# Kernel tuning notes

Hardware: AMD Instinct MI355X
Metric: run time of the kernel (lower is better)

The kernel has to match this reference:

```python
import jax, jax.numpy as jnp
import numpy as np

D = 1024
H = 16
HD = D // H
B = 4
L = 2048
FFN = 4 * D
EPS = 1e-5


def _layer_norm(x, g, b):
    mu = jnp.mean(x, axis=-1, keepdims=True)
    var = jnp.mean(jnp.square(x - mu), axis=-1, keepdims=True)
    return (x - mu) * jax.lax.rsqrt(var + EPS) * g + b


def setup_inputs() -> dict:
    key = jax.random.key(0)
    ks = jax.random.split(key, 16)
    s = 1.0 / np.sqrt(D)
    inp = {
        "x": jax.random.normal(ks[0], (B, L, D), dtype=jnp.float32),
        "rel_pos_bias": jax.random.normal(ks[1], (1, H, L, L), dtype=jnp.float32) * 0.02,
        "wq": jax.random.normal(ks[2], (D, D), dtype=jnp.float32) * s,
        "bq": jnp.zeros((D,), jnp.float32),
        "wk": jax.random.normal(ks[3], (D, D), dtype=jnp.float32) * s,
        "bk": jnp.zeros((D,), jnp.float32),
        "wv": jax.random.normal(ks[4], (D, D), dtype=jnp.float32) * s,
        "bv": jnp.zeros((D,), jnp.float32),
        "wo": jax.random.normal(ks[5], (D, D), dtype=jnp.float32) * s,
        "bo": jnp.zeros((D,), jnp.float32),
        "g1": jnp.ones((D,), jnp.float32),
        "be1": jnp.zeros((D,), jnp.float32),
        "g2": jnp.ones((D,), jnp.float32),
        "be2": jnp.zeros((D,), jnp.float32),
        "w1": jax.random.normal(ks[6], (D, FFN), dtype=jnp.float32) * s,
        "bf1": jnp.zeros((FFN,), jnp.float32),
        "w2": jax.random.normal(ks[7], (FFN, D), dtype=jnp.float32) * (1.0 / np.sqrt(FFN)),
        "bf2": jnp.zeros((D,), jnp.float32),
    }
    return inp


def reference(x, rel_pos_bias, wq, bq, wk, bk, wv, bv, wo, bo,
              g1, be1, g2, be2, w1, bf1, w2, bf2):
    scale = HD ** -0.5
    residual = x
    xn = _layer_norm(x, g1, be1)
    # projections -> (B, H, L, HD)
    q = (xn @ wq + bq).reshape(B, L, H, HD).transpose(0, 2, 1, 3)
    k = (xn @ wk + bk).reshape(B, L, H, HD).transpose(0, 2, 1, 3)
    v = (xn @ wv + bv).reshape(B, L, H, HD).transpose(0, 2, 1, 3)
    scores = jnp.einsum('bhqd,bhkd->bhqk', q, k) * scale
    causal = jnp.tril(jnp.ones((L, L), dtype=bool))
    scores = jnp.where(causal[None, None], scores, -jnp.inf)
    scores = scores + rel_pos_bias
    attn = jax.nn.softmax(scores, axis=-1)
    out = jnp.einsum('bhqk,bhkd->bhqd', attn, v)
    out = out.transpose(0, 2, 1, 3).reshape(B, L, D)
    out = out @ wo + bo
    x = residual + out
    residual = x
    xn = _layer_norm(x, g2, be2)
    h = jax.nn.relu(xn @ w1 + bf1)
    x = residual + (h @ w2 + bf2)
    return x
```

## Files before the change

### kernel.cpp

```cpp
#include <hip/hip_runtime.h>
#include <hip/hip_bf16.h>

#define D_   1024
#define H_   16
#define HD_  64
#define B_   4
#define L_   2048
#define FFN_ 4096
#define M_   (B_ * L_)

typedef __bf16 bf16x8 __attribute__((ext_vector_type(8)));
typedef float f32x4 __attribute__((ext_vector_type(4)));
typedef unsigned short ushort8 __attribute__((ext_vector_type(8)));
typedef unsigned short ushort4v __attribute__((ext_vector_type(4)));

__device__ inline unsigned short f2bf(float f) {
    unsigned int u = __float_as_uint(f);
    u += 0x7fff + ((u >> 16) & 1);
    return (unsigned short)(u >> 16);
}
__device__ inline float bf2f(unsigned short u) {
    return __uint_as_float(((unsigned int)u) << 16);
}

__global__ __launch_bounds__(256) void k_transpose_bf16(
    const float* __restrict__ in, unsigned short* __restrict__ out, int K, int N)
{
    __shared__ float tile[64][65];
    int k0 = blockIdx.y * 64, n0 = blockIdx.x * 64;
    int t = threadIdx.x;
    int r = t >> 2, cs = (t & 3) * 16;
    const float* src = in + (size_t)(k0 + r) * N + n0 + cs;
#pragma unroll
    for (int i = 0; i < 16; i += 4) {
        float4 v = *(const float4*)(src + i);
        tile[r][cs + i + 0] = v.x;
        tile[r][cs + i + 1] = v.y;
        tile[r][cs + i + 2] = v.z;
        tile[r][cs + i + 3] = v.w;
    }
    __syncthreads();
    unsigned short* dst = out + (size_t)(n0 + r) * K + k0 + cs;
#pragma unroll
    for (int i = 0; i < 16; ++i) dst[i] = f2bf(tile[cs + i][r]);
}

__global__ void k_concat_bias(const float* __restrict__ bq, const float* __restrict__ bk,
                              const float* __restrict__ bv, float* __restrict__ out)
{
    int i = blockIdx.x * 256 + threadIdx.x;
    float v = (i < 1024) ? bq[i] : (i < 2048 ? bk[i - 1024] : bv[i - 2048]);
    out[i] = v;
}

__global__ __launch_bounds__(256) void k_layernorm(
    const float* __restrict__ x, const float* __restrict__ g, const float* __restrict__ be,
    unsigned short* __restrict__ out)
{
    int row = blockIdx.x;
    const float* xr = x + (size_t)row * D_;
    int t = threadIdx.x;
    float4 v = *(const float4*)(xr + t * 4);
    float s = v.x + v.y + v.z + v.w;
    float sq = v.x * v.x + v.y * v.y + v.z * v.z + v.w * v.w;
#pragma unroll
    for (int off = 32; off >= 1; off >>= 1) {
        s  += __shfl_down(s, off);
        sq += __shfl_down(sq, off);
    }
    __shared__ float ps[4], psq[4];
    int w = t >> 6;
    if ((t & 63) == 0) { ps[w] = s; psq[w] = sq; }
    __syncthreads();
    float tot  = ps[0] + ps[1] + ps[2] + ps[3];
    float totq = psq[0] + psq[1] + psq[2] + psq[3];
    float mu  = tot * (1.f / D_);
    float var = totq * (1.f / D_) - mu * mu;
    float inv = rsqrtf(var + 1e-5f);
    float4 gv = *(const float4*)(g + t * 4);
    float4 bv = *(const float4*)(be + t * 4);
    ushort4v o;
    o[0] = f2bf((v.x - mu) * inv * gv.x + bv.x);
    o[1] = f2bf((v.y - mu) * inv * gv.y + bv.y);
    o[2] = f2bf((v.z - mu) * inv * gv.z + bv.z);
    o[3] = f2bf((v.w - mu) * inv * gv.w + bv.w);
    *(ushort4v*)(out + (size_t)row * D_ + t * 4) = o;
}

template <bool OUT_BF16, bool RELU, bool RESID>
__global__ __launch_bounds__(256, 2) void k_gemm(
    const unsigned short* __restrict__ A, const unsigned short* __restrict__ Bt,
    const float* __restrict__ bias, const float* __restrict__ resid,
    void* __restrict__ Cout, int M, int N, int K)
{
    __shared__ unsigned short sA[128 * 40];
    __shared__ unsigned short sB[128 * 40];
    int m0 = blockIdx.y * 128, n0 = blockIdx.x * 128;
    int tid = threadIdx.x, lane = tid & 63, wvi = tid >> 6;
    int wm = (wvi & 1) * 64, wn = (wvi >> 1) * 64;
    int lr = lane & 15, qd = lane >> 4;

    f32x4 acc[4][4] = {};

    int sr = tid >> 2, ss = (tid & 3) * 8;
    const unsigned short* pA0 = A  + (size_t)(m0 + sr)      * K + ss;
    const unsigned short* pA1 = A  + (size_t)(m0 + 64 + sr) * K + ss;
    const unsigned short* pB0 = Bt + (size_t)(n0 + sr)      * K + ss;
    const unsigned short* pB1 = Bt + (size_t)(n0 + 64 + sr) * K + ss;

    for (int k0 = 0; k0 < K; k0 += 32) {
        ushort8 a0 = *(const ushort8*)(pA0 + k0);
        ushort8 a1 = *(const ushort8*)(pA1 + k0);
        ushort8 b0 = *(const ushort8*)(pB0 + k0);
        ushort8 b1 = *(const ushort8*)(pB1 + k0);
        if (k0) __syncthreads();
        *(ushort8*)(sA + sr * 40 + ss)        = a0;
        *(ushort8*)(sA + (64 + sr) * 40 + ss) = a1;
        *(ushort8*)(sB + sr * 40 + ss)        = b0;
        *(ushort8*)(sB + (64 + sr) * 40 + ss) = b1;
        __syncthreads();
        bf16x8 af[4], bfr[4];
#pragma unroll
        for (int i = 0; i < 4; ++i)
            af[i] = *(const bf16x8*)(sA + (wm + i * 16 + lr) * 40 + qd * 8);
#pragma unroll
        for (int i = 0; i < 4; ++i)
            bfr[i] = *(const bf16x8*)(sB + (wn + i * 16 + lr) * 40 + qd * 8);
#pragma unroll
        for (int mi = 0; mi < 4; ++mi)
#pragma unroll
            for (int ni = 0; ni < 4; ++ni)
                acc[mi][ni] = __builtin_amdgcn_mfma_f32_16x16x32_bf16(
                    af[mi], bfr[ni], acc[mi][ni], 0, 0, 0);
    }

#pragma unroll
    for (int ni = 0; ni < 4; ++ni) {
        int col = n0 + wn + ni * 16 + lr;
        float bvv = bias[col];
#pragma unroll
        for (int mi = 0; mi < 4; ++mi) {
#pragma unroll
            for (int r = 0; r < 4; ++r) {
                int row = m0 + wm + mi * 16 + qd * 4 + r;
                float v = acc[mi][ni][r] + bvv;
                if (RELU) v = fmaxf(v, 0.f);
                if (RESID) v += resid[(size_t)row * N + col];
                if (OUT_BF16)
                    ((unsigned short*)Cout)[(size_t)row * N + col] = f2bf(v);
                else
                    ((float*)Cout)[(size_t)row * N + col] = v;
            }
        }
    }
}

__global__ __launch_bounds__(256, 2) void k_attn(
    const unsigned short* __restrict__ qkv, const float* __restrict__ rpb,
    unsigned short* __restrict__ out)
{
    __shared__ unsigned short Qs[64 * 72];
    __shared__ unsigned short Ks[64 * 72];
    __shared__ unsigned short Vt[64 * 72];
    __shared__ unsigned short Sp[64 * 72];
    int h = blockIdx.x >> 2, b = blockIdx.x & 3;
    int q0 = blockIdx.y * 64;
    int t = threadIdx.x, lane = t & 63, w = t >> 6;
    int lr = lane & 15, qd = lane >> 4;
    int sr = t >> 2, ss = (t & 3) * 16;

    {
        const unsigned short* src = qkv + (size_t)(b * L_ + q0 + sr) * 3072 + h * 64 + ss;
        *(ushort8*)(Qs + sr * 72 + ss)     = *(const ushort8*)src;
        *(ushort8*)(Qs + sr * 72 + ss + 8) = *(const ushort8*)(src + 8);
    }

    f32x4 oacc[4] = {};
    float m_r[4], l_r[4];
#pragma unroll
    for (int r = 0; r < 4; ++r) { m_r[r] = -1e30f; l_r[r] = 0.f; }

    int ntile = q0 / 64 + 1;
    for (int kt = 0; kt < ntile; ++kt) {
        int k0 = kt * 64;
        __syncthreads();
        const unsigned short* ksrc = qkv + (size_t)(b * L_ + k0 + sr) * 3072 + 1024 + h * 64 + ss;
        *(ushort8*)(Ks + sr * 72 + ss)     = *(const ushort8*)ksrc;
        *(ushort8*)(Ks + sr * 72 + ss + 8) = *(const ushort8*)(ksrc + 8);
        const unsigned short* vsrc = qkv + (size_t)(b * L_ + k0 + sr) * 3072 + 2048 + h * 64 + ss;
        ushort8 v0 = *(const ushort8*)vsrc;
        ushort8 v1 = *(const ushort8*)(vsrc + 8);
#pragma unroll
        for (int i = 0; i < 8; ++i) Vt[(ss + i) * 72 + sr] = v0[i];
#pragma unroll
        for (int i = 0; i < 8; ++i) Vt[(ss + 8 + i) * 72 + sr] = v1[i];
        __syncthreads();

        f32x4 sc[4] = {};
#pragma unroll
        for (int ks = 0; ks < 2; ++ks) {
            bf16x8 aq = *(const bf16x8*)(Qs + (w * 16 + lr) * 72 + ks * 32 + qd * 8);
#pragma unroll
            for (int nt = 0; nt < 4; ++nt) {
                bf16x8 bk8 = *(const bf16x8*)(Ks + (nt * 16 + lr) * 72 + ks * 32 + qd * 8);
                sc[nt] = __builtin_amdgcn_mfma_f32_16x16x32_bf16(aq, bk8, sc[nt], 0, 0, 0);
            }
        }

        int qrow_base = q0 + w * 16 + qd * 4;
        const float* rpb_base = rpb + ((size_t)h * L_ + qrow_base) * L_ + k0;
        float pvv[4][4], mx[4];
#pragma unroll
        for (int r = 0; r < 4; ++r) {
            mx[r] = -1e30f;
#pragma unroll
            for (int nt = 0; nt < 4; ++nt) {
                int kcol = k0 + nt * 16 + lr;
                float sv = sc[nt][r] * 0.125f + rpb_base[(size_t)r * L_ + nt * 16 + lr];
                if (kcol > qrow_base + r) sv = -1e30f;
                pvv[r][nt] = sv;
                mx[r] = fmaxf(mx[r], sv);
            }
        }
#pragma unroll
        for (int r = 0; r < 4; ++r) {
            mx[r] = fmaxf(mx[r], __shfl_xor(mx[r], 1));
            mx[r] = fmaxf(mx[r], __shfl_xor(mx[r], 2));
            mx[r] = fmaxf(mx[r], __shfl_xor(mx[r], 4));
            mx[r] = fmaxf(mx[r], __shfl_xor(mx[r], 8));
        }
#pragma unroll
        for (int r = 0; r < 4; ++r) {
            float mnew  = fmaxf(m_r[r], mx[r]);
            float alpha = __expf(m_r[r] - mnew);
            float psum = 0.f;
#pragma unroll
            for (int nt = 0; nt < 4; ++nt) {
                float p = __expf(pvv[r][nt] - mnew);
                psum += p;
                Sp[(w * 16 + qd * 4 + r) * 72 + nt * 16 + lr] = f2bf(p);
            }
            psum += __shfl_xor(psum, 1);
            psum += __shfl_xor(psum, 2);
            psum += __shfl_xor(psum, 4);
            psum += __shfl_xor(psum, 8);
            l_r[r] = l_r[r] * alpha + psum;
            m_r[r] = mnew;
            oacc[0][r] *= alpha; oacc[1][r] *= alpha;
            oacc[2][r] *= alpha; oacc[3][r] *= alpha;
        }

#pragma unroll
        for (int ks = 0; ks < 2; ++ks) {
            bf16x8 ap = *(const bf16x8*)(Sp + (w * 16 + lr) * 72 + ks * 32 + qd * 8);
#pragma unroll
            for (int dt = 0; dt < 4; ++dt) {
                bf16x8 bv8 = *(const bf16x8*)(Vt + (dt * 16 + lr) * 72 + ks * 32 + qd * 8);
                oacc[dt] = __builtin_amdgcn_mfma_f32_16x16x32_bf16(ap, bv8, oacc[dt], 0, 0, 0);
            }
        }
    }

#pragma unroll
    for (int r = 0; r < 4; ++r) {
        float linv = 1.f / l_r[r];
        int qrow = q0 + w * 16 + qd * 4 + r;
        unsigned short* dst = out + (size_t)(b * L_ + qrow) * 1024 + h * 64;
#pragma unroll
        for (int dt = 0; dt < 4; ++dt)
            dst[dt * 16 + lr] = f2bf(oacc[dt][r] * linv);
    }
}

extern "C" void kernel_launch(void* const* d_in, const int* in_sizes, int n_in,
                              void* d_out, int out_size, void* d_ws, size_t ws_size,
                              hipStream_t stream)
{
    const float* x   = (const float*)d_in[0];
    const float* rpb = (const float*)d_in[1];
    const float* wq  = (const float*)d_in[2];
    const float* bq  = (const float*)d_in[3];
    const float* wk  = (const float*)d_in[4];
    const float* bk  = (const float*)d_in[5];
    const float* wv  = (const float*)d_in[6];
    const float* bv  = (const float*)d_in[7];
    const float* wo  = (const float*)d_in[8];
    const float* bo  = (const float*)d_in[9];
    const float* g1  = (const float*)d_in[10];
    const float* be1 = (const float*)d_in[11];
    const float* g2  = (const float*)d_in[12];
    const float* be2 = (const float*)d_in[13];
    const float* w1  = (const float*)d_in[14];
    const float* bf1 = (const float*)d_in[15];
    const float* w2  = (const float*)d_in[16];
    const float* bf2 = (const float*)d_in[17];
    float* out = (float*)d_out;
    char* ws = (char*)d_ws;

    unsigned short* xn1   = (unsigned short*)(ws + 0);
    unsigned short* qkv   = (unsigned short*)(ws + 16777216);
    unsigned short* attno = (unsigned short*)(ws + 0);
    unsigned short* hbuf  = (unsigned short*)(ws + 0);
    float*          xmid  = (float*)(ws + 67108864);
    unsigned short* xn2   = (unsigned short*)(ws + 100663296);
    unsigned short* wqkvT = (unsigned short*)(ws + 117440512);
    unsigned short* woT   = (unsigned short*)(ws + 123731968);
    unsigned short* w1T   = (unsigned short*)(ws + 125829120);
    unsigned short* w2T   = (unsigned short*)(ws + 134217728);
    float*          bqkv  = (float*)(ws + 142606336);

    k_transpose_bf16<<<dim3(16, 16), 256, 0, stream>>>(wq, wqkvT,                1024, 1024);
    k_transpose_bf16<<<dim3(16, 16), 256, 0, stream>>>(wk, wqkvT + 1024 * 1024,  1024, 1024);
    k_transpose_bf16<<<dim3(16, 16), 256, 0, stream>>>(wv, wqkvT + 2048 * 1024,  1024, 1024);
    k_transpose_bf16<<<dim3(16, 16), 256, 0, stream>>>(wo, woT,                  1024, 1024);
    k_transpose_bf16<<<dim3(64, 16), 256, 0, stream>>>(w1, w1T,                  1024, 4096);
    k_transpose_bf16<<<dim3(16, 64), 256, 0, stream>>>(w2, w2T,                  4096, 1024);
    k_concat_bias<<<12, 256, 0, stream>>>(bq, bk, bv, bqkv);

    k_layernorm<<<M_, 256, 0, stream>>>(x, g1, be1, xn1);
    k_gemm<true, false, false><<<dim3(24, 64), 256, 0, stream>>>(
        xn1, wqkvT, bqkv, nullptr, qkv, M_, 3072, 1024);
    k_attn<<<dim3(64, 32), 256, 0, stream>>>(qkv, rpb, attno);
    k_gemm<false, false, true><<<dim3(8, 64), 256, 0, stream>>>(
        attno, woT, bo, x, xmid, M_, 1024, 1024);
    k_layernorm<<<M_, 256, 0, stream>>>(xmid, g2, be2, xn2);
    k_gemm<true, true, false><<<dim3(32, 64), 256, 0, stream>>>(
        xn2, w1T, bf1, nullptr, hbuf, M_, 4096, 1024);
    k_gemm<false, false, true><<<dim3(8, 64), 256, 0, stream>>>(
        hbuf, w2T, bf2, xmid, out, M_, 1024, 4096);
}
```

Baseline: 1.023 ms.

## Restructure attention to share bias across batches; direct-to-LDS GEMM loads

The attention kernel now runs one 512-thread block per head and query tile, with its eight waves spread over the four batches. The relative-position-bias rows are therefore read by all batches together and can be reused from cache. Q, K and V fragments are loaded straight from global memory into registers instead of being staged in LDS, and query tiles run heaviest-first to balance the causal work. The QKV GEMM epilogue now writes V already transposed, removing the scalar LDS transpose inside attention. The GEMM mainloop uses global_load_lds to fill shared memory directly with unpadded 32-wide rows, which may add LDS bank conflicts on the fragment reads.

```diff
diff --git a/kernel.cpp b/kernel.cpp
--- a/kernel.cpp
+++ b/kernel.cpp
@@ -19,8 +19,16 @@
     u += 0x7fff + ((u >> 16) & 1);
     return (unsigned short)(u >> 16);
 }
-__device__ inline float bf2f(unsigned short u) {
-    return __uint_as_float(((unsigned int)u) << 16);
+
+__device__ __forceinline__ void gll16(const unsigned short* g, unsigned short* lbase) {
+#if defined(__has_builtin) && __has_builtin(__builtin_amdgcn_global_load_lds)
+    __builtin_amdgcn_global_load_lds(
+        (const __attribute__((address_space(1))) unsigned int*)g,
+        (__attribute__((address_space(3))) unsigned int*)lbase, 16, 0, 0);
+#else
+    int l = threadIdx.x & 63;
+    *(ushort8*)(lbase + l * 8) = *(const ushort8*)g;
+#endif
 }
 
 __global__ __launch_bounds__(256) void k_transpose_bf16(
@@ -87,45 +95,47 @@
     *(ushort4v*)(out + (size_t)row * D_ + t * 4) = o;
 }
 
-template <bool OUT_BF16, bool RELU, bool RESID>
+template <int EPI>
 __global__ __launch_bounds__(256, 2) void k_gemm(
     const unsigned short* __restrict__ A, const unsigned short* __restrict__ Bt,
     const float* __restrict__ bias, const float* __restrict__ resid,
-    void* __restrict__ Cout, int M, int N, int K)
-{
-    __shared__ unsigned short sA[128 * 40];
-    __shared__ unsigned short sB[128 * 40];
+    void* __restrict__ out0, unsigned short* __restrict__ vT,
+    int M, int N, int K)
+{
+    __shared__ unsigned short sA[128 * 32];
+    __shared__ unsigned short sB[128 * 32];
     int m0 = blockIdx.y * 128, n0 = blockIdx.x * 128;
-    int tid = threadIdx.x, lane = tid & 63, wvi = tid >> 6;
-    int wm = (wvi & 1) * 64, wn = (wvi >> 1) * 64;
+    int tid = threadIdx.x, lane = tid & 63, w = tid >> 6;
+    int wm = (w & 1) * 64, wn = (w >> 1) * 64;
     int lr = lane & 15, qd = lane >> 4;
 
+    int srow = w * 32 + (lane >> 2);
+    int scol = (lane & 3) * 8;
+    const unsigned short* gA0 = A  + (size_t)(m0 + srow) * K + scol;
+    const unsigned short* gA1 = A  + (size_t)(m0 + srow + 16) * K + scol;
+    const unsigned short* gB0 = Bt + (size_t)(n0 + srow) * K + scol;
+    const unsigned short* gB1 = Bt + (size_t)(n0 + srow + 16) * K + scol;
+    unsigned short* lA0 = sA + w * 1024;
+    unsigned short* lA1 = sA + w * 1024 + 512;
+    unsigned short* lB0 = sB + w * 1024;
+    unsigned short* lB1 = sB + w * 1024 + 512;
+
     f32x4 acc[4][4] = {};
 
-    int sr = tid >> 2, ss = (tid & 3) * 8;
-    const unsigned short* pA0 = A  + (size_t)(m0 + sr)      * K + ss;
-    const unsigned short* pA1 = A  + (size_t)(m0 + 64 + sr) * K + ss;
-    const unsigned short* pB0 = Bt + (size_t)(n0 + sr)      * K + ss;
-    const unsigned short* pB1 = Bt + (size_t)(n0 + 64 + sr) * K + ss;
-
     for (int k0 = 0; k0 < K; k0 += 32) {
-        ushort8 a0 = *(const ushort8*)(pA0 + k0);
-        ushort8 a1 = *(const ushort8*)(pA1 + k0);
-        ushort8 b0 = *(const ushort8*)(pB0 + k0);
-        ushort8 b1 = *(const ushort8*)(pB1 + k0);
         if (k0) __syncthreads();
-        *(ushort8*)(sA + sr * 40 + ss)        = a0;
-        *(ushort8*)(sA + (64 + sr) * 40 + ss) = a1;
-        *(ushort8*)(sB + sr * 40 + ss)        = b0;
-        *(ushort8*)(sB + (64 + sr) * 40 + ss) = b1;
+        gll16(gA0 + k0, lA0);
+        gll16(gA1 + k0, lA1);
+        gll16(gB0 + k0, lB0);
+        gll16(gB1 + k0, lB1);
         __syncthreads();
         bf16x8 af[4], bfr[4];
 #pragma unroll
         for (int i = 0; i < 4; ++i)
-            af[i] = *(const bf16x8*)(sA + (wm + i * 16 + lr) * 40 + qd * 8);
+            af[i] = *(const bf16x8*)(sA + (wm + i * 16 + lr) * 32 + qd * 8);
 #pragma unroll
         for (int i = 0; i < 4; ++i)
-            bfr[i] = *(const bf16x8*)(sB + (wn + i * 16 + lr) * 40 + qd * 8);
+            bfr[i] = *(const bf16x8*)(sB + (wn + i * 16 + lr) * 32 + qd * 8);
 #pragma unroll
         for (int mi = 0; mi < 4; ++mi)
 #pragma unroll
@@ -140,136 +150,158 @@
         float bvv = bias[col];
 #pragma unroll
         for (int mi = 0; mi < 4; ++mi) {
-#pragma unroll
-            for (int r = 0; r < 4; ++r) {
-                int row = m0 + wm + mi * 16 + qd * 4 + r;
-                float v = acc[mi][ni][r] + bvv;
-                if (RELU) v = fmaxf(v, 0.f);
-                if (RESID) v += resid[(size_t)row * N + col];
-                if (OUT_BF16)
-                    ((unsigned short*)Cout)[(size_t)row * N + col] = f2bf(v);
-                else
-                    ((float*)Cout)[(size_t)row * N + col] = v;
+            int row0 = m0 + wm + mi * 16 + qd * 4;
+            if (EPI == 3 && col >= 2048) {
+                int b = row0 >> 11, key = row0 & 2047;
+                int hd = col - 2048;
+                ushort4v pk;
+#pragma unroll
+                for (int r = 0; r < 4; ++r) pk[r] = f2bf(acc[mi][ni][r] + bvv);
+                *(ushort4v*)(vT + ((size_t)(b * 1024 + hd)) * 2048 + key) = pk;
+            } else {
+#pragma unroll
+                for (int r = 0; r < 4; ++r) {
+                    float v = acc[mi][ni][r] + bvv;
+                    if (EPI == 2) v = fmaxf(v, 0.f);
+                    if (EPI == 0) {
+                        v += resid[(size_t)(row0 + r) * N + col];
+                        ((float*)out0)[(size_t)(row0 + r) * N + col] = v;
+                    } else if (EPI == 3) {
+                        ((unsigned short*)out0)[(size_t)(row0 + r) * 2048 + col] = f2bf(v);
+                    } else {
+                        ((unsigned short*)out0)[(size_t)(row0 + r) * N + col] = f2bf(v);
+                    }
+                }
             }
         }
     }
 }
 
-__global__ __launch_bounds__(256, 2) void k_attn(
-    const unsigned short* __restrict__ qkv, const float* __restrict__ rpb,
-    unsigned short* __restrict__ out)
-{
-    __shared__ unsigned short Qs[64 * 72];
-    __shared__ unsigned short Ks[64 * 72];
-    __shared__ unsigned short Vt[64 * 72];
-    __shared__ unsigned short Sp[64 * 72];
-    int h = blockIdx.x >> 2, b = blockIdx.x & 3;
-    int q0 = blockIdx.y * 64;
-    int t = threadIdx.x, lane = t & 63, w = t >> 6;
+__global__ __launch_bounds__(512, 2) void k_attn(
+    const unsigned short* __restrict__ qk, const unsigned short* __restrict__ vT,
+    const float* __restrict__ rpb, unsigned short* __restrict__ attno)
+{
+    __shared__ unsigned short Sp[8 * 32 * 72];
+    int h = blockIdx.x;
+    int qt = 31 - blockIdx.y;
+    int q0 = qt * 64;
+    int tid = threadIdx.x, lane = tid & 63, w = tid >> 6;
+    int b = w & 3, half = w >> 2;
     int lr = lane & 15, qd = lane >> 4;
-    int sr = t >> 2, ss = (t & 3) * 16;
-
-    {
-        const unsigned short* src = qkv + (size_t)(b * L_ + q0 + sr) * 3072 + h * 64 + ss;
-        *(ushort8*)(Qs + sr * 72 + ss)     = *(const ushort8*)src;
-        *(ushort8*)(Qs + sr * 72 + ss + 8) = *(const ushort8*)(src + 8);
-    }
-
-    f32x4 oacc[4] = {};
-    float m_r[4], l_r[4];
-#pragma unroll
-    for (int r = 0; r < 4; ++r) { m_r[r] = -1e30f; l_r[r] = 0.f; }
-
-    int ntile = q0 / 64 + 1;
-    for (int kt = 0; kt < ntile; ++kt) {
+    unsigned short* sp = Sp + w * (32 * 72);
+
+    const unsigned short* qkb = qk + (size_t)b * 2048 * 2048;
+    const unsigned short* vb  = vT + ((size_t)(b * 1024 + h * 64)) * 2048;
+    const float* rpbh = rpb + (size_t)h * 2048 * 2048;
+
+    bf16x8 qf[2][2];
+#pragma unroll
+    for (int mi = 0; mi < 2; ++mi)
+#pragma unroll
+        for (int ks = 0; ks < 2; ++ks)
+            qf[mi][ks] = *(const bf16x8*)(qkb +
+                (size_t)(q0 + half * 32 + mi * 16 + lr) * 2048 + h * 64 + ks * 32 + qd * 8);
+
+    f32x4 o[2][4] = {};
+    float m_s[2][4], l_s[2][4];
+#pragma unroll
+    for (int mi = 0; mi < 2; ++mi)
+#pragma unroll
+        for (int r = 0; r < 4; ++r) { m_s[mi][r] = -1e30f; l_s[mi][r] = 0.f; }
+
+    for (int kt = 0; kt <= qt; ++kt) {
         int k0 = kt * 64;
-        __syncthreads();
-        const unsigned short* ksrc = qkv + (size_t)(b * L_ + k0 + sr) * 3072 + 1024 + h * 64 + ss;
-        *(ushort8*)(Ks + sr * 72 + ss)     = *(const ushort8*)ksrc;
-        *(ushort8*)(Ks + sr * 72 + ss + 8) = *(const ushort8*)(ksrc + 8);
-        const unsigned short* vsrc = qkv + (size_t)(b * L_ + k0 + sr) * 3072 + 2048 + h * 64 + ss;
-        ushort8 v0 = *(const ushort8*)vsrc;
-        ushort8 v1 = *(const ushort8*)(vsrc + 8);
-#pragma unroll
-        for (int i = 0; i < 8; ++i) Vt[(ss + i) * 72 + sr] = v0[i];
-#pragma unroll
-        for (int i = 0; i < 8; ++i) Vt[(ss + 8 + i) * 72 + sr] = v1[i];
-        __syncthreads();
-
-        f32x4 sc[4] = {};
-#pragma unroll
-        for (int ks = 0; ks < 2; ++ks) {
-            bf16x8 aq = *(const bf16x8*)(Qs + (w * 16 + lr) * 72 + ks * 32 + qd * 8);
-#pragma unroll
-            for (int nt = 0; nt < 4; ++nt) {
-                bf16x8 bk8 = *(const bf16x8*)(Ks + (nt * 16 + lr) * 72 + ks * 32 + qd * 8);
-                sc[nt] = __builtin_amdgcn_mfma_f32_16x16x32_bf16(aq, bk8, sc[nt], 0, 0, 0);
+        bf16x8 kf[4][2];
+#pragma unroll
+        for (int nt = 0; nt < 4; ++nt)
+#pragma unroll
+            for (int ks = 0; ks < 2; ++ks)
+                kf[nt][ks] = *(const bf16x8*)(qkb +
+                    (size_t)(k0 + nt * 16 + lr) * 2048 + 1024 + h * 64 + ks * 32 + qd * 8);
+
+        f32x4 sc[2][4] = {};
+#pragma unroll
+        for (int ks = 0; ks < 2; ++ks)
+#pragma unroll
+            for (int mi = 0; mi < 2; ++mi)
+#pragma unroll
+                for (int nt = 0; nt < 4; ++nt)
+                    sc[mi][nt] = __builtin_amdgcn_mfma_f32_16x16x32_bf16(
+                        qf[mi][ks], kf[nt][ks], sc[mi][nt], 0, 0, 0);
+
+        bool diag = (kt == qt);
+#pragma unroll
+        for (int mi = 0; mi < 2; ++mi) {
+            int qr0 = q0 + half * 32 + mi * 16 + qd * 4;
+#pragma unroll
+            for (int r = 0; r < 4; ++r) {
+                const float* rp = rpbh + (size_t)(qr0 + r) * 2048 + k0;
+                float e[4], mx = -1e30f;
+#pragma unroll
+                for (int nt = 0; nt < 4; ++nt) {
+                    float sv = sc[mi][nt][r] * 0.125f + rp[nt * 16 + lr];
+                    if (diag && (k0 + nt * 16 + lr > qr0 + r)) sv = -1e30f;
+                    e[nt] = sv;
+                    mx = fmaxf(mx, sv);
+                }
+                mx = fmaxf(mx, __shfl_xor(mx, 1));
+                mx = fmaxf(mx, __shfl_xor(mx, 2));
+                mx = fmaxf(mx, __shfl_xor(mx, 4));
+                mx = fmaxf(mx, __shfl_xor(mx, 8));
+                float mnew = fmaxf(m_s[mi][r], mx);
+                float al = __expf(m_s[mi][r] - mnew);
+                float ps = 0.f;
+#pragma unroll
+                for (int nt = 0; nt < 4; ++nt) {
+                    float p = __expf(e[nt] - mnew);
+                    ps += p;
+                    sp[(mi * 16 + qd * 4 + r) * 72 + nt * 16 + lr] = f2bf(p);
+                }
+                ps += __shfl_xor(ps, 1);
+                ps += __shfl_xor(ps, 2);
+                ps += __shfl_xor(ps, 4);
+                ps += __shfl_xor(ps, 8);
+                l_s[mi][r] = l_s[mi][r] * al + ps;
+                m_s[mi][r] = mnew;
+#pragma unroll
+                for (int dt = 0; dt < 4; ++dt) o[mi][dt][r] *= al;
             }
         }
 
-        int qrow_base = q0 + w * 16 + qd * 4;
-        const float* rpb_base = rpb + ((size_t)h * L_ + qrow_base) * L_ + k0;
-        float pvv[4][4], mx[4];
+        bf16x8 vf[4][2];
+#pragma unroll
+        for (int dt = 0; dt < 4; ++dt)
+#pragma unroll
+            for (int ks = 0; ks < 2; ++ks)
+                vf[dt][ks] = *(const bf16x8*)(vb +
+                    (size_t)(dt * 16 + lr) * 2048 + k0 + ks * 32 + qd * 8);
+        bf16x8 ap[2][2];
+#pragma unroll
+        for (int mi = 0; mi < 2; ++mi)
+#pragma unroll
+            for (int ks = 0; ks < 2; ++ks)
+                ap[mi][ks] = *(const bf16x8*)(sp + (mi * 16 + lr) * 72 + ks * 32 + qd * 8);
+#pragma unroll
+        for (int ks = 0; ks < 2; ++ks)
+#pragma unroll
+            for (int mi = 0; mi < 2; ++mi)
+#pragma unroll
+                for (int dt = 0; dt < 4; ++dt)
+                    o[mi][dt] = __builtin_amdgcn_mfma_f32_16x16x32_bf16(
+                        ap[mi][ks], vf[dt][ks], o[mi][dt], 0, 0, 0);
+    }
+
+#pragma unroll
+    for (int mi = 0; mi < 2; ++mi)
 #pragma unroll
         for (int r = 0; r < 4; ++r) {
-            mx[r] = -1e30f;
-#pragma unroll
-            for (int nt = 0; nt < 4; ++nt) {
-                int kcol = k0 + nt * 16 + lr;
-                float sv = sc[nt][r] * 0.125f + rpb_base[(size_t)r * L_ + nt * 16 + lr];
-                if (kcol > qrow_base + r) sv = -1e30f;
-                pvv[r][nt] = sv;
-                mx[r] = fmaxf(mx[r], sv);
-            }
+            float linv = 1.f / l_s[mi][r];
+            int qrow = q0 + half * 32 + mi * 16 + qd * 4 + r;
+            unsigned short* dst = attno + ((size_t)(b * 2048 + qrow)) * 1024 + h * 64;
+#pragma unroll
+            for (int dt = 0; dt < 4; ++dt)
+                dst[dt * 16 + lr] = f2bf(o[mi][dt][r] * linv);
         }
-#pragma unroll
-        for (int r = 0; r < 4; ++r) {
-            mx[r] = fmaxf(mx[r], __shfl_xor(mx[r], 1));
-            mx[r] = fmaxf(mx[r], __shfl_xor(mx[r], 2));
-            mx[r] = fmaxf(mx[r], __shfl_xor(mx[r], 4));
-            mx[r] = fmaxf(mx[r], __shfl_xor(mx[r], 8));
-        }
-#pragma unroll
-        for (int r = 0; r < 4; ++r) {
-            float mnew  = fmaxf(m_r[r], mx[r]);
-            float alpha = __expf(m_r[r] - mnew);
-            float psum = 0.f;
-#pragma unroll
-            for (int nt = 0; nt < 4; ++nt) {
-                float p = __expf(pvv[r][nt] - mnew);
-                psum += p;
-                Sp[(w * 16 + qd * 4 + r) * 72 + nt * 16 + lr] = f2bf(p);
-            }
-            psum += __shfl_xor(psum, 1);
-            psum += __shfl_xor(psum, 2);
-            psum += __shfl_xor(psum, 4);
-            psum += __shfl_xor(psum, 8);
-            l_r[r] = l_r[r] * alpha + psum;
-            m_r[r] = mnew;
-            oacc[0][r] *= alpha; oacc[1][r] *= alpha;
-            oacc[2][r] *= alpha; oacc[3][r] *= alpha;
-        }
-
-#pragma unroll
-        for (int ks = 0; ks < 2; ++ks) {
-            bf16x8 ap = *(const bf16x8*)(Sp + (w * 16 + lr) * 72 + ks * 32 + qd * 8);
-#pragma unroll
-            for (int dt = 0; dt < 4; ++dt) {
-                bf16x8 bv8 = *(const bf16x8*)(Vt + (dt * 16 + lr) * 72 + ks * 32 + qd * 8);
-                oacc[dt] = __builtin_amdgcn_mfma_f32_16x16x32_bf16(ap, bv8, oacc[dt], 0, 0, 0);
-            }
-        }
-    }
-
-#pragma unroll
-    for (int r = 0; r < 4; ++r) {
-        float linv = 1.f / l_r[r];
-        int qrow = q0 + w * 16 + qd * 4 + r;
-        unsigned short* dst = out + (size_t)(b * L_ + qrow) * 1024 + h * 64;
-#pragma unroll
-        for (int dt = 0; dt < 4; ++dt)
-            dst[dt * 16 + lr] = f2bf(oacc[dt][r] * linv);
-    }
 }
 
 extern "C" void kernel_launch(void* const* d_in, const int* in_sizes, int n_in,
@@ -298,9 +330,10 @@
     char* ws = (char*)d_ws;
 
     unsigned short* xn1   = (unsigned short*)(ws + 0);
-    unsigned short* qkv   = (unsigned short*)(ws + 16777216);
     unsigned short* attno = (unsigned short*)(ws + 0);
     unsigned short* hbuf  = (unsigned short*)(ws + 0);
+    unsigned short* qk    = (unsigned short*)(ws + 16777216);
+    unsigned short* vT    = (unsigned short*)(ws + 50331648);
     float*          xmid  = (float*)(ws + 67108864);
     unsigned short* xn2   = (unsigned short*)(ws + 100663296);
     unsigned short* wqkvT = (unsigned short*)(ws + 117440512);
@@ -309,23 +342,23 @@
     unsigned short* w2T   = (unsigned short*)(ws + 134217728);
     float*          bqkv  = (float*)(ws + 142606336);
 
-    k_transpose_bf16<<<dim3(16, 16), 256, 0, stream>>>(wq, wqkvT,                1024, 1024);
-    k_transpose_bf16<<<dim3(16, 16), 256, 0, stream>>>(wk, wqkvT + 1024 * 1024,  1024, 1024);
-    k_transpose_bf16<<<dim3(16, 16), 256, 0, stream>>>(wv, wqkvT + 2048 * 1024,  1024, 1024);
-    k_transpose_bf16<<<dim3(16, 16), 256, 0, stream>>>(wo, woT,                  1024, 1024);
-    k_transpose_bf16<<<dim3(64, 16), 256, 0, stream>>>(w1, w1T,                  1024, 4096);
-    k_transpose_bf16<<<dim3(16, 64), 256, 0, stream>>>(w2, w2T,                  4096, 1024);
+    k_transpose_bf16<<<dim3(16, 16), 256, 0, stream>>>(wq, wqkvT,               1024, 1024);
+    k_transpose_bf16<<<dim3(16, 16), 256, 0, stream>>>(wk, wqkvT + 1024 * 1024, 1024, 1024);
+    k_transpose_bf16<<<dim3(16, 16), 256, 0, stream>>>(wv, wqkvT + 2048 * 1024, 1024, 1024);
+    k_transpose_bf16<<<dim3(16, 16), 256, 0, stream>>>(wo, woT,                 1024, 1024);
+    k_transpose_bf16<<<dim3(64, 16), 256, 0, stream>>>(w1, w1T,                 1024, 4096);
+    k_transpose_bf16<<<dim3(16, 64), 256, 0, stream>>>(w2, w2T,                 4096, 1024);
     k_concat_bias<<<12, 256, 0, stream>>>(bq, bk, bv, bqkv);
 
     k_layernorm<<<M_, 256, 0, stream>>>(x, g1, be1, xn1);
-    k_gemm<true, false, false><<<dim3(24, 64), 256, 0, stream>>>(
-        xn1, wqkvT, bqkv, nullptr, qkv, M_, 3072, 1024);
-    k_attn<<<dim3(64, 32), 256, 0, stream>>>(qkv, rpb, attno);
-    k_gemm<false, false, true><<<dim3(8, 64), 256, 0, stream>>>(
-        attno, woT, bo, x, xmid, M_, 1024, 1024);
+    k_gemm<3><<<dim3(24, 64), 256, 0, stream>>>(
+        xn1, wqkvT, bqkv, nullptr, qk, vT, M_, 3072, 1024);
+    k_attn<<<dim3(16, 32), 512, 0, stream>>>(qk, vT, rpb, attno);
+    k_gemm<0><<<dim3(8, 64), 256, 0, stream>>>(
+        attno, woT, bo, x, xmid, nullptr, M_, 1024, 1024);
     k_layernorm<<<M_, 256, 0, stream>>>(xmid, g2, be2, xn2);
-    k_gemm<true, true, false><<<dim3(32, 64), 256, 0, stream>>>(
-        xn2, w1T, bf1, nullptr, hbuf, M_, 4096, 1024);
-    k_gemm<false, false, true><<<dim3(8, 64), 256, 0, stream>>>(
-        hbuf, w2T, bf2, xmid, out, M_, 1024, 4096);
-}
+    k_gemm<2><<<dim3(32, 64), 256, 0, stream>>>(
+        xn2, w1T, bf1, nullptr, hbuf, nullptr, M_, 4096, 1024);
+    k_gemm<0><<<dim3(8, 64), 256, 0, stream>>>(
+        hbuf, w2T, bf2, xmid, out, nullptr, M_, 1024, 4096);
+}
```

Measured after the change: 1.086 ms. 1.06x slower.
